# Kernel optimization log

Measured on AMD Instinct MI355X. Metric: run time of the kernel, lower is better.

The kernel has to match this reference:

```python
import jax, jax.numpy as jnp
import numpy as np

N_RAYS = 8192
AABB_LO, AABB_HI = -1.5, 1.5
GRID = 300
STEP_RATIO = 3.0
DIST_SCALE = 25.0
W_THRES = 1e-4
NEAR, FAR = 0.05, 6.0
NUM_SEM, DIM_INST = 20, 16
H_DEN, H_APP, F_APP, F_SEM = 64, 64, 27, 32

_EXT = AABB_HI - AABB_LO
STEP_SIZE = (_EXT / (GRID - 1 + 0.001)) * STEP_RATIO          # update_step_size
N_SAMPLES = int(np.sqrt(3.0) * _EXT / STEP_SIZE) + 1          # 173


def setup_inputs() -> dict:
    key = jax.random.key(0)
    ks = jax.random.split(key, 12)
    o = jax.random.normal(ks[0], (N_RAYS, 3), jnp.float32)
    o = 4.0 * o / jnp.linalg.norm(o, axis=-1, keepdims=True)      # camera origins on radius-4 sphere
    tgt = jax.random.uniform(ks[1], (N_RAYS, 3), jnp.float32, minval=-0.5, maxval=0.5)
    d = tgt - o
    d = d / jnp.linalg.norm(d, axis=-1, keepdims=True)            # unit viewdirs through the box
    rays = jnp.concatenate([o, d], -1)
    g = lambda k, shp, fan: jax.random.normal(k, shp, jnp.float32) / np.sqrt(fan)
    return {
        'rays': rays,
        'Wd1': g(ks[2], (3, H_DEN), 3), 'bd1': jnp.zeros((H_DEN,), jnp.float32),
        'Wd2': g(ks[3], (H_DEN, 1), H_DEN), 'bd2': jnp.zeros((1,), jnp.float32),
        'Wapp': g(ks[4], (3, F_APP), 3),
        'Wa1': g(ks[5], (F_APP + 3, H_APP), F_APP + 3), 'ba1': jnp.zeros((H_APP,), jnp.float32),
        'Wa2': g(ks[6], (H_APP, 3), H_APP), 'ba2': jnp.zeros((3,), jnp.float32),
        'Wsf': g(ks[7], (3, F_SEM), 3),
        'Wsm': g(ks[8], (F_SEM, NUM_SEM), F_SEM), 'bsm': jnp.zeros((NUM_SEM,), jnp.float32),
        'Wi': g(ks[9], (3, DIM_INST), 3),
        'perturb': 0, 'white_bg': 1, 'is_train': 0,
    }


def _render(rays, Wd1, bd1, Wd2, bd2, Wapp, Wa1, ba1, Wa2, ba2, Wsf, Wsm, bsm, Wi,
            white_bg):
    lo = jnp.full((3,), AABB_LO, rays.dtype)
    hi = jnp.full((3,), AABB_HI, rays.dtype)
    o, d = rays[:, :3], rays[:, 3:6]
    # --- sample_points_in_box (TensoRF sample_ray, perturb=0) ---
    vec = jnp.where(d == 0, 1e-6, d)
    rate_a = (hi - o) / vec
    rate_b = (lo - o) / vec
    t_min = jnp.clip(jnp.minimum(rate_a, rate_b).max(-1), NEAR, FAR)       # [N]
    rng = jnp.arange(N_SAMPLES, dtype=rays.dtype)
    z_vals = t_min[:, None] + rng[None, :] * STEP_SIZE                     # [N,S]
    xyz = o[:, None, :] + d[:, None, :] * z_vals[..., None]                # [N,S,3]
    mask_xyz = jnp.all((xyz >= lo) & (xyz <= hi), -1)                      # [N,S]
    dists = jnp.concatenate([z_vals[:, 1:] - z_vals[:, :-1],
                             jnp.zeros_like(z_vals[:, :1])], -1)
    mid = jnp.concatenate([(z_vals[:, 1:] + z_vals[:, :-1]) * 0.5,
                           z_vals[:, -2:-1]], -1)
    # --- normalize_coordinates ---
    xyzn = (xyz - lo) * (2.0 / _EXT) - 1.0
    # --- density (masked query -> dense compute + where, same values) ---
    h = jax.nn.relu(xyzn @ Wd1 + bd1)                                      # [N,S,Hd]
    sigma = jnp.where(mask_xyz, jax.nn.softplus((h @ Wd2 + bd2)[..., 0]), 0.0)
    # --- raw_to_alpha ---
    alpha = 1.0 - jnp.exp(-sigma * (dists * DIST_SCALE))                   # [N,S]
    T = jnp.cumprod(jnp.concatenate([jnp.ones_like(alpha[:, :1]),
                                     1.0 - alpha + 1e-10], -1), -1)
    weight = alpha * T[:, :-1]
    # --- eff_distloss(weight, mid, dists) ---
    loss_uni = (dists * weight * weight).sum(-1).mean() / 3.0
    wm = weight * mid
    w_cs = jnp.cumsum(weight, -1)
    wm_cs = jnp.cumsum(wm, -1)
    loss_bi = 2.0 * (wm[:, 1:] * w_cs[:, :-1] - weight[:, 1:] * wm_cs[:, :-1]).sum(-1).mean()
    dist_reg = loss_uni + loss_bi
    # --- appearance / semantics / instances on appearance_mask ---
    app_mask = weight > W_THRES
    viewdirs = jnp.broadcast_to(d[:, None, :], xyz.shape)
    feat = xyzn @ Wapp                                                     # [N,S,27]
    ha = jax.nn.relu(jnp.concatenate([feat, viewdirs], -1) @ Wa1 + ba1)    # [N,S,Ha]
    rgb = jnp.where(app_mask[..., None], jax.nn.sigmoid(ha @ Wa2 + ba2), 0.0)
    sem = jnp.where(app_mask[..., None], (xyzn @ Wsf) @ Wsm + bsm, 0.0)
    inst = jnp.where(app_mask[..., None], xyzn @ Wi, 0.0)
    # --- compositing ---
    opacity = weight.sum(-1)
    rgb_map = (weight[..., None] * rgb).sum(-2)
    depth_map = (weight * z_vals).sum(-1)
    w = jax.lax.stop_gradient(weight)[..., None]                           # stop_semantic_grad
    semantics = (w * sem).sum(-2)
    instances = (w * inst).sum(-2)                                          # is_train=False
    if white_bg:
        rgb_map = rgb_map + (1.0 - opacity[..., None])
    rgb_map = jnp.clip(rgb_map, 0.0, 1.0)
    return rgb_map, semantics, instances, depth_map, dist_reg


def reference(rays, Wd1, bd1, Wd2, bd2, Wapp, Wa1, ba1, Wa2, ba2, Wsf, Wsm, bsm, Wi,
              perturb, white_bg, is_train):
    return _render(rays, Wd1, bd1, Wd2, bd2, Wapp, Wa1, ba1, Wa2, ba2,
                   Wsf, Wsm, bsm, Wi, bool(white_bg))
```

## Files before the change

kernel.cpp:

```cpp
#include <hip/hip_runtime.h>

#define NRAYS 8192
#define NSAMP 173
#define LASTI 172
#define NBLK  (NRAYS / 4)

__device__ __forceinline__ float RL(float x, int u) {
    return __int_as_float(__builtin_amdgcn_readlane(__float_as_int(x), u));
}

template <int CTRL, int RM, bool BC>
__device__ __forceinline__ float updpp(float old, float x) {
    return __int_as_float(__builtin_amdgcn_update_dpp(
        __float_as_int(old), __float_as_int(x), CTRL, RM, 0xf, BC));
}

__device__ __forceinline__ float scan_add64(float x) {
    x += updpp<0x111, 0xf, true>(0.f, x);
    x += updpp<0x112, 0xf, true>(0.f, x);
    x += updpp<0x114, 0xf, true>(0.f, x);
    x += updpp<0x118, 0xf, true>(0.f, x);
    x += updpp<0x142, 0xa, true>(0.f, x);
    x += updpp<0x143, 0xc, true>(0.f, x);
    return x;
}

__device__ __forceinline__ float scan_mul64(float x) {
    x *= updpp<0x111, 0xf, false>(1.f, x);
    x *= updpp<0x112, 0xf, false>(1.f, x);
    x *= updpp<0x114, 0xf, false>(1.f, x);
    x *= updpp<0x118, 0xf, false>(1.f, x);
    x *= updpp<0x142, 0xa, false>(1.f, x);
    x *= updpp<0x143, 0xc, false>(1.f, x);
    return x;
}

__device__ __forceinline__ float wave_sum64(float v) {
    return RL(scan_add64(v), 63);
}

__device__ __forceinline__ float softplus_f(float x) {
    if (x > 15.f) return x;
    return __logf(1.f + __expf(x));
}
__device__ __forceinline__ float sigmoid_f(float x) {
    return 1.f / (1.f + __expf(-x));
}

__launch_bounds__(256, 4)
__global__ void render_kernel(
    const float* __restrict__ rays,
    const float* __restrict__ Wd1, const float* __restrict__ bd1,
    const float* __restrict__ Wd2, const float* __restrict__ bd2,
    const float* __restrict__ Wapp, const float* __restrict__ Wa1,
    const float* __restrict__ ba1, const float* __restrict__ Wa2,
    const float* __restrict__ ba2, const float* __restrict__ Wsf,
    const float* __restrict__ Wsm, const float* __restrict__ bsm,
    const float* __restrict__ Wi,
    const int* __restrict__ whitebg_p,
    float* __restrict__ out,
    float* __restrict__ wsdist)
{
    __shared__ float4 qd4[64];
    __shared__ float  wd2s[64];
    __shared__ float4 apAs[64];
    __shared__ float2 apBs[64];
    __shared__ float  wscs[60];
    __shared__ float  bsmS[20];

    const int t = threadIdx.x;
    const int wid = t >> 6, lane = t & 63;
    const int r = blockIdx.x * 4 + wid;

    if (t < 64) {
        qd4[t] = make_float4(Wd1[t], Wd1[64 + t], Wd1[128 + t], bd1[t]);
        wd2s[t] = Wd2[t];
    } else if (t < 128) {
        int u = t - 64;
        apBs[u] = make_float2(Wa2[3 * u + 1], Wa2[3 * u + 2]);
    } else if (t < 192) {
        int u = t - 128;
        float s0 = 0.f, s1 = 0.f, s2 = 0.f;
        for (int j = 0; j < 27; ++j) {
            float w = Wa1[j * 64 + u];
            s0 = fmaf(Wapp[j], w, s0);
            s1 = fmaf(Wapp[27 + j], w, s1);
            s2 = fmaf(Wapp[54 + j], w, s2);
        }
        apAs[u] = make_float4(s0, s1, s2, Wa2[3 * u]);
    } else {
        for (int job = t - 192; job < 80; job += 64) {
            if (job < 60) {
                int m = job / 20, s = job % 20;
                float a = 0.f;
                for (int k = 0; k < 32; ++k) a = fmaf(Wsf[m * 32 + k], Wsm[k * 20 + s], a);
                wscs[job] = a;
            } else {
                bsmS[job - 60] = bsm[job - 60];
            }
        }
    }

    const float o0 = rays[r * 6 + 0], o1 = rays[r * 6 + 1], o2 = rays[r * 6 + 2];
    const float d0 = rays[r * 6 + 3], d1 = rays[r * 6 + 4], d2 = rays[r * 6 + 5];

    float tm;
    {
        float v0 = (d0 == 0.f) ? 1e-6f : d0;
        float v1 = (d1 == 0.f) ? 1e-6f : d1;
        float v2 = (d2 == 0.f) ? 1e-6f : d2;
        float a0 = __fdiv_rn(__fsub_rn(1.5f, o0), v0), b0 = __fdiv_rn(__fsub_rn(-1.5f, o0), v0);
        float a1 = __fdiv_rn(__fsub_rn(1.5f, o1), v1), b1 = __fdiv_rn(__fsub_rn(-1.5f, o1), v1);
        float a2 = __fdiv_rn(__fsub_rn(1.5f, o2), v2), b2 = __fdiv_rn(__fsub_rn(-1.5f, o2), v2);
        float m0 = fminf(a0, b0), m1 = fminf(a1, b1), m2 = fminf(a2, b2);
        tm = fmaxf(fmaxf(m0, m1), m2);
        tm = fminf(fmaxf(tm, 0.05f), 6.0f);
    }

    float dcr;
    {
        float b = ba1[lane];
        b = fmaf(d0, Wa1[27 * 64 + lane], b);
        b = fmaf(d1, Wa1[28 * 64 + lane], b);
        b = fmaf(d2, Wa1[29 * 64 + lane], b);
        dcr = b;
    }

    const float bd2c = bd2[0];
    const float ba2c0 = ba2[0], ba2c1 = ba2[1], ba2c2 = ba2[2];

    __syncthreads();

    const float STEPF = (float)(3.0 / 299.001 * 3.0);
    const float zlast2 = __fadd_rn(tm, __fmul_rn(171.f, STEPF));

    float aR0 = 0.f, aR1 = 0.f, aR2 = 0.f;
    float aS0 = 0.f, aS1 = 0.f, aS2 = 0.f;
    float aSw = 0.f;
    float aD = 0.f, aLu = 0.f, aLb = 0.f;
    float Tc = 1.f, Wcar = 0.f, WMc = 0.f;

    for (int c = 0; c < 3; ++c) {
        int i = (c << 6) + lane;
        bool valid = i < NSAMP;
        float z = __fadd_rn(tm, __fmul_rn((float)i, STEPF));
        float x0 = __fadd_rn(o0, __fmul_rn(d0, z));
        float x1 = __fadd_rn(o1, __fmul_rn(d1, z));
        float x2 = __fadd_rn(o2, __fmul_rn(d2, z));
        bool inbox = valid && (x0 >= -1.5f) && (x0 <= 1.5f) && (x1 >= -1.5f) && (x1 <= 1.5f) &&
                     (x2 >= -1.5f) && (x2 <= 1.5f);
        if (__ballot(inbox) == 0ull) break;

        float xn0 = x0 * (2.f / 3.f), xn1 = x1 * (2.f / 3.f), xn2 = x2 * (2.f / 3.f);

        float sp = bd2c;
#pragma unroll 8
        for (int u = 0; u < 64; ++u) {
            float4 q = qd4[u];
            float h = fmaf(xn0, q.x, fmaf(xn1, q.y, fmaf(xn2, q.z, q.w)));
            sp = fmaf(fmaxf(h, 0.f), wd2s[u], sp);
        }
        float sigma = inbox ? softplus_f(sp) : 0.f;

        float znext = __fadd_rn(tm, __fmul_rn((float)(i + 1), STEPF));
        float dist = (i < LASTI) ? __fsub_rn(znext, z) : 0.f;
        float alpha = 1.f - __expf(-sigma * dist * 25.f);
        float f = 1.f - alpha + 1e-10f;

        float p = scan_mul64(f);
        float pex = updpp<0x138, 0xf, false>(1.f, p);
        float T = Tc * pex;
        float w = alpha * T;

        float mid = (i < LASTI) ? 0.5f * __fadd_rn(z, znext) : zlast2;
        float wm = w * mid;

        float sw = scan_add64(w);
        float swm = scan_add64(wm);
        float wex = updpp<0x138, 0xf, true>(0.f, sw);
        float wmex = updpp<0x138, 0xf, true>(0.f, swm);

        aLb += wm * (Wcar + wex) - w * (WMc + wmex);
        aLu = fmaf(dist * w, w, aLu);
        aD = fmaf(w, z, aD);

        Tc *= RL(p, 63);
        Wcar += RL(sw, 63);
        WMc += RL(swm, 63);

        float wapp = (w > 1e-4f) ? w : 0.f;
        if (__ballot(wapp > 0.f) != 0ull) {
            float c0 = 0.f, c1 = 0.f, c2 = 0.f;
#pragma unroll 8
            for (int u = 0; u < 64; ++u) {
                float4 A4 = apAs[u];
                float2 B2 = apBs[u];
                float dcu = RL(dcr, u);
                float h = fmaf(xn0, A4.x, fmaf(xn1, A4.y, fmaf(xn2, A4.z, dcu)));
                h = fmaxf(h, 0.f);
                c0 = fmaf(h, A4.w, c0);
                c1 = fmaf(h, B2.x, c1);
                c2 = fmaf(h, B2.y, c2);
            }
            aR0 = fmaf(wapp, sigmoid_f(c0 + ba2c0), aR0);
            aR1 = fmaf(wapp, sigmoid_f(c1 + ba2c1), aR1);
            aR2 = fmaf(wapp, sigmoid_f(c2 + ba2c2), aR2);
            aS0 = fmaf(wapp, xn0, aS0);
            aS1 = fmaf(wapp, xn1, aS1);
            aS2 = fmaf(wapp, xn2, aS2);
            aSw += wapp;
        }

        if (Tc < 1e-8f) break;
    }

    aR0 = wave_sum64(aR0); aR1 = wave_sum64(aR1); aR2 = wave_sum64(aR2);
    aS0 = wave_sum64(aS0); aS1 = wave_sum64(aS1); aS2 = wave_sum64(aS2);
    aSw = wave_sum64(aSw);
    aD = wave_sum64(aD);
    aLu = wave_sum64(aLu);
    aLb = wave_sum64(aLb);

    float opac = Wcar;
    int wb = *whitebg_p;
    float bg = wb ? (1.f - opac) : 0.f;

    float* out_rgb = out;
    float* out_sem = out + 24576;
    float* out_inst = out + 188416;
    float* out_dep = out + 319488;

    if (lane < 3) {
        float rv = (lane == 0 ? aR0 : (lane == 1 ? aR1 : aR2)) + bg;
        rv = fminf(fmaxf(rv, 0.f), 1.f);
        out_rgb[r * 3 + lane] = rv;
    }
    if (lane < 20) {
        float sv = aS0 * wscs[lane] + aS1 * wscs[20 + lane] + aS2 * wscs[40 + lane] +
                   aSw * bsmS[lane];
        out_sem[r * 20 + lane] = sv;
    }
    if (lane < 16) {
        float iv = aS0 * Wi[lane] + aS1 * Wi[16 + lane] + aS2 * Wi[32 + lane];
        out_inst[r * 16 + lane] = iv;
    }
    if (lane == 0) {
        out_dep[r] = aD;
        wsdist[r] = aLu * (1.f / 3.f) + 2.f * aLb;
    }
}

__global__ void reduce_dist_kernel(const float* __restrict__ ws, float* __restrict__ out) {
    __shared__ float sm[256];
    int t = threadIdx.x;
    float a = 0.f;
    const float4* w4 = (const float4*)ws;
    for (int i = t; i < NRAYS / 4; i += 256) {
        float4 v = w4[i];
        a += (v.x + v.y) + (v.z + v.w);
    }
    sm[t] = a;
    __syncthreads();
    for (int st = 128; st > 0; st >>= 1) {
        if (t < st) sm[t] += sm[t + st];
        __syncthreads();
    }
    if (t == 0) out[0] = sm[0] * (1.f / (float)NRAYS);
}

extern "C" void kernel_launch(void* const* d_in, const int* in_sizes, int n_in,
                              void* d_out, int out_size, void* d_ws, size_t ws_size,
                              hipStream_t stream) {
    const float* rays = (const float*)d_in[0];
    const float* Wd1  = (const float*)d_in[1];
    const float* bd1  = (const float*)d_in[2];
    const float* Wd2  = (const float*)d_in[3];
    const float* bd2  = (const float*)d_in[4];
    const float* Wapp = (const float*)d_in[5];
    const float* Wa1  = (const float*)d_in[6];
    const float* ba1  = (const float*)d_in[7];
    const float* Wa2  = (const float*)d_in[8];
    const float* ba2  = (const float*)d_in[9];
    const float* Wsf  = (const float*)d_in[10];
    const float* Wsm  = (const float*)d_in[11];
    const float* bsm  = (const float*)d_in[12];
    const float* Wi   = (const float*)d_in[13];
    const int* wb     = (const int*)d_in[15];

    float* out = (float*)d_out;
    float* wsd = (float*)d_ws;

    render_kernel<<<NBLK, 256, 0, stream>>>(rays, Wd1, bd1, Wd2, bd2, Wapp, Wa1, ba1,
                                            Wa2, ba2, Wsf, Wsm, bsm, Wi, wb, out, wsd);
    reduce_dist_kernel<<<1, 256, 0, stream>>>(wsd, out + 327680);
}
```

Measured before the change: 29.25 us.

## Fold ray origin and direction into per-ray linear coefficients for MLP hidden units

Since sample points lie on a ray, each first-layer hidden pre-activation is affine in z. The kernel now precomputes a per-wave slope and intercept for every hidden unit, for both the density MLP and the appearance MLP, and stores them in per-wave shared arrays. The inner loops then need one FMA per hidden unit instead of three, and the readlane broadcast goes away. The cost is an extra per-ray setup phase, larger shared memory, and slightly different floating-point rounding.

```diff
diff --git a/kernel.cpp b/kernel.cpp
--- a/kernel.cpp
+++ b/kernel.cpp
@@ -61,10 +61,10 @@
     float* __restrict__ out,
     float* __restrict__ wsdist)
 {
-    __shared__ float4 qd4[64];
-    __shared__ float  wd2s[64];
+    __shared__ float4 gkwD[4][64];
+    __shared__ float2 gkA[4][64];
+    __shared__ float4 bQ[64];
     __shared__ float4 apAs[64];
-    __shared__ float2 apBs[64];
     __shared__ float  wscs[60];
     __shared__ float  bsmS[20];
 
@@ -73,12 +73,8 @@
     const int r = blockIdx.x * 4 + wid;
 
     if (t < 64) {
-        qd4[t] = make_float4(Wd1[t], Wd1[64 + t], Wd1[128 + t], bd1[t]);
-        wd2s[t] = Wd2[t];
-    } else if (t < 128) {
-        int u = t - 64;
-        apBs[u] = make_float2(Wa2[3 * u + 1], Wa2[3 * u + 2]);
-    } else if (t < 192) {
+        bQ[t] = make_float4(Wa2[3 * t], Wa2[3 * t + 1], Wa2[3 * t + 2], 0.f);
+    } else if (t >= 128 && t < 192) {
         int u = t - 128;
         float s0 = 0.f, s1 = 0.f, s2 = 0.f;
         for (int j = 0; j < 27; ++j) {
@@ -87,8 +83,8 @@
             s1 = fmaf(Wapp[27 + j], w, s1);
             s2 = fmaf(Wapp[54 + j], w, s2);
         }
-        apAs[u] = make_float4(s0, s1, s2, Wa2[3 * u]);
-    } else {
+        apAs[u] = make_float4(s0, s1, s2, 0.f);
+    } else if (t >= 192) {
         for (int job = t - 192; job < 80; job += 64) {
             if (job < 60) {
                 int m = job / 20, s = job % 20;
@@ -117,19 +113,29 @@
         tm = fminf(fmaxf(tm, 0.05f), 6.0f);
     }
 
-    float dcr;
     {
-        float b = ba1[lane];
-        b = fmaf(d0, Wa1[27 * 64 + lane], b);
-        b = fmaf(d1, Wa1[28 * 64 + lane], b);
-        b = fmaf(d2, Wa1[29 * 64 + lane], b);
-        dcr = b;
+        float qx = Wd1[lane], qy = Wd1[64 + lane], qz = Wd1[128 + lane];
+        float qw = bd1[lane], w2 = Wd2[lane];
+        float gd = fmaf(d2, qz, fmaf(d1, qy, d0 * qx)) * (2.f / 3.f);
+        float kd = fmaf(fmaf(o2, qz, fmaf(o1, qy, o0 * qx)), (2.f / 3.f), qw);
+        gkwD[wid][lane] = make_float4(gd, kd, w2, 0.f);
     }
 
     const float bd2c = bd2[0];
     const float ba2c0 = ba2[0], ba2c1 = ba2[1], ba2c2 = ba2[2];
 
     __syncthreads();
+
+    {
+        float4 A = apAs[lane];
+        float dc = ba1[lane];
+        dc = fmaf(d0, Wa1[27 * 64 + lane], dc);
+        dc = fmaf(d1, Wa1[28 * 64 + lane], dc);
+        dc = fmaf(d2, Wa1[29 * 64 + lane], dc);
+        float ga = fmaf(d2, A.z, fmaf(d1, A.y, d0 * A.x)) * (2.f / 3.f);
+        float ka = fmaf(fmaf(o2, A.z, fmaf(o1, A.y, o0 * A.x)), (2.f / 3.f), dc);
+        gkA[wid][lane] = make_float2(ga, ka);
+    }
 
     const float STEPF = (float)(3.0 / 299.001 * 3.0);
     const float zlast2 = __fadd_rn(tm, __fmul_rn(171.f, STEPF));
@@ -156,9 +162,9 @@
         float sp = bd2c;
 #pragma unroll 8
         for (int u = 0; u < 64; ++u) {
-            float4 q = qd4[u];
-            float h = fmaf(xn0, q.x, fmaf(xn1, q.y, fmaf(xn2, q.z, q.w)));
-            sp = fmaf(fmaxf(h, 0.f), wd2s[u], sp);
+            float4 g = gkwD[wid][u];
+            float h = fmaf(z, g.x, g.y);
+            sp = fmaf(fmaxf(h, 0.f), g.z, sp);
         }
         float sigma = inbox ? softplus_f(sp) : 0.f;
 
@@ -193,14 +199,13 @@
             float c0 = 0.f, c1 = 0.f, c2 = 0.f;
 #pragma unroll 8
             for (int u = 0; u < 64; ++u) {
-                float4 A4 = apAs[u];
-                float2 B2 = apBs[u];
-                float dcu = RL(dcr, u);
-                float h = fmaf(xn0, A4.x, fmaf(xn1, A4.y, fmaf(xn2, A4.z, dcu)));
+                float2 g = gkA[wid][u];
+                float4 b = bQ[u];
+                float h = fmaf(z, g.x, g.y);
                 h = fmaxf(h, 0.f);
-                c0 = fmaf(h, A4.w, c0);
-                c1 = fmaf(h, B2.x, c1);
-                c2 = fmaf(h, B2.y, c2);
+                c0 = fmaf(h, b.x, c0);
+                c1 = fmaf(h, b.y, c1);
+                c2 = fmaf(h, b.z, c2);
             }
             aR0 = fmaf(wapp, sigmoid_f(c0 + ba2c0), aR0);
             aR1 = fmaf(wapp, sigmoid_f(c1 + ba2c1), aR1);
```

Result: slower. 32.49 us (+11.1%).

## Keep MLP weights in registers and broadcast via DPP row_newbcast inline asm

Applied to the files above, without the earlier changes.

Each lane now holds a 16-way slice of the density and appearance MLP weights in VGPRs, loaded once per wave. The per-sample hidden units are computed with v_fmac_f32_dpp row_newbcast, which broadcasts one register lane per row, replacing per-iteration LDS reads of weights and per-unit readlane of the direction bias. This removes LDS traffic and SGPR readlane serialization from the inner loops. The cost is more VGPRs, four partial accumulators that change summation order, and reliance on gfx950-specific DPP modes written in inline assembly.

```diff
diff --git a/kernel.cpp b/kernel.cpp
--- a/kernel.cpp
+++ b/kernel.cpp
@@ -46,6 +46,43 @@
 __device__ __forceinline__ float sigmoid_f(float x) {
     return 1.f / (1.f + __expf(-x));
 }
+
+#define RMASK " row_mask:0xf bank_mask:0xf"
+
+#define DEN1(S, N)                                                                    \
+    do {                                                                              \
+        float t_;                                                                     \
+        asm("v_mov_b32_dpp %[t], %[qw] row_newbcast:" #N RMASK "\n\t"                 \
+            "v_fmac_f32_dpp %[t], %[qx], %[x0] row_newbcast:" #N RMASK "\n\t"         \
+            "v_fmac_f32_dpp %[t], %[qy], %[x1] row_newbcast:" #N RMASK "\n\t"         \
+            "v_fmac_f32_dpp %[t], %[qz], %[x2] row_newbcast:" #N RMASK "\n\t"         \
+            "v_max_f32 %[t], 0, %[t]\n\t"                                             \
+            "v_fmac_f32_dpp %[sp], %[w2], %[t] row_newbcast:" #N RMASK                \
+            : [t] "=&v"(t_), [sp] "+v"(sps##S)                                        \
+            : [qw] "v"(qw[S]), [qx] "v"(qx[S]), [qy] "v"(qy[S]), [qz] "v"(qz[S]),     \
+              [w2] "v"(w2[S]), [x0] "v"(xn0), [x1] "v"(xn1), [x2] "v"(xn2));          \
+    } while (0)
+
+#define DEN4(N) DEN1(0, N); DEN1(1, N); DEN1(2, N); DEN1(3, N)
+
+#define APP1(S, N)                                                                    \
+    do {                                                                              \
+        float t_;                                                                     \
+        asm("v_mov_b32_dpp %[t], %[dcv] row_newbcast:" #N RMASK "\n\t"                \
+            "v_fmac_f32_dpp %[t], %[a0], %[x0] row_newbcast:" #N RMASK "\n\t"         \
+            "v_fmac_f32_dpp %[t], %[a1], %[x1] row_newbcast:" #N RMASK "\n\t"         \
+            "v_fmac_f32_dpp %[t], %[a2], %[x2] row_newbcast:" #N RMASK "\n\t"         \
+            "v_max_f32 %[t], 0, %[t]\n\t"                                             \
+            "v_fmac_f32_dpp %[c0], %[b0], %[t] row_newbcast:" #N RMASK "\n\t"         \
+            "v_fmac_f32_dpp %[c1], %[b1], %[t] row_newbcast:" #N RMASK "\n\t"         \
+            "v_fmac_f32_dpp %[c2], %[b2], %[t] row_newbcast:" #N RMASK                \
+            : [t] "=&v"(t_), [c0] "+v"(c0##S), [c1] "+v"(c1##S), [c2] "+v"(c2##S)     \
+            : [dcv] "v"(dc[S]), [a0] "v"(a0r[S]), [a1] "v"(a1r[S]), [a2] "v"(a2r[S]), \
+              [b0] "v"(b0r[S]), [b1] "v"(b1r[S]), [b2] "v"(b2r[S]),                   \
+              [x0] "v"(xn0), [x1] "v"(xn1), [x2] "v"(xn2));                           \
+    } while (0)
+
+#define APP4(N) APP1(0, N); APP1(1, N); APP1(2, N); APP1(3, N)
 
 __launch_bounds__(256, 4)
 __global__ void render_kernel(
@@ -70,6 +107,7 @@
 
     const int t = threadIdx.x;
     const int wid = t >> 6, lane = t & 63;
+    const int k = lane & 15;
     const int r = blockIdx.x * 4 + wid;
 
     if (t < 64) {
@@ -93,7 +131,7 @@
             if (job < 60) {
                 int m = job / 20, s = job % 20;
                 float a = 0.f;
-                for (int k = 0; k < 32; ++k) a = fmaf(Wsf[m * 32 + k], Wsm[k * 20 + s], a);
+                for (int kk = 0; kk < 32; ++kk) a = fmaf(Wsf[m * 32 + kk], Wsm[kk * 20 + s], a);
                 wscs[job] = a;
             } else {
                 bsmS[job - 60] = bsm[job - 60];
@@ -117,19 +155,29 @@
         tm = fminf(fmaxf(tm, 0.05f), 6.0f);
     }
 
-    float dcr;
-    {
-        float b = ba1[lane];
-        b = fmaf(d0, Wa1[27 * 64 + lane], b);
-        b = fmaf(d1, Wa1[28 * 64 + lane], b);
-        b = fmaf(d2, Wa1[29 * 64 + lane], b);
-        dcr = b;
-    }
-
     const float bd2c = bd2[0];
     const float ba2c0 = ba2[0], ba2c1 = ba2[1], ba2c2 = ba2[2];
 
     __syncthreads();
+
+    float qx[4], qy[4], qz[4], qw[4], w2[4];
+    float dc[4], a0r[4], a1r[4], a2r[4], b0r[4], b1r[4], b2r[4];
+#pragma unroll
+    for (int s = 0; s < 4; ++s) {
+        int idx = 16 * s + k;
+        float4 q = qd4[idx];
+        qx[s] = q.x; qy[s] = q.y; qz[s] = q.z; qw[s] = q.w;
+        w2[s] = wd2s[idx];
+        float4 A = apAs[idx];
+        a0r[s] = A.x; a1r[s] = A.y; a2r[s] = A.z; b0r[s] = A.w;
+        float2 B = apBs[idx];
+        b1r[s] = B.x; b2r[s] = B.y;
+        float b = ba1[idx];
+        b = fmaf(d0, Wa1[27 * 64 + idx], b);
+        b = fmaf(d1, Wa1[28 * 64 + idx], b);
+        b = fmaf(d2, Wa1[29 * 64 + idx], b);
+        dc[s] = b;
+    }
 
     const float STEPF = (float)(3.0 / 299.001 * 3.0);
     const float zlast2 = __fadd_rn(tm, __fmul_rn(171.f, STEPF));
@@ -153,14 +201,13 @@
 
         float xn0 = x0 * (2.f / 3.f), xn1 = x1 * (2.f / 3.f), xn2 = x2 * (2.f / 3.f);
 
-        float sp = bd2c;
-#pragma unroll 8
-        for (int u = 0; u < 64; ++u) {
-            float4 q = qd4[u];
-            float h = fmaf(xn0, q.x, fmaf(xn1, q.y, fmaf(xn2, q.z, q.w)));
-            sp = fmaf(fmaxf(h, 0.f), wd2s[u], sp);
-        }
-        float sigma = inbox ? softplus_f(sp) : 0.f;
+        float sps0 = bd2c, sps1 = 0.f, sps2 = 0.f, sps3 = 0.f;
+        DEN4(0);  DEN4(1);  DEN4(2);  DEN4(3);
+        DEN4(4);  DEN4(5);  DEN4(6);  DEN4(7);
+        DEN4(8);  DEN4(9);  DEN4(10); DEN4(11);
+        DEN4(12); DEN4(13); DEN4(14); DEN4(15);
+        float spv = (sps0 + sps1) + (sps2 + sps3);
+        float sigma = inbox ? softplus_f(spv) : 0.f;
 
         float znext = __fadd_rn(tm, __fmul_rn((float)(i + 1), STEPF));
         float dist = (i < LASTI) ? __fsub_rn(znext, z) : 0.f;
@@ -190,21 +237,19 @@
 
         float wapp = (w > 1e-4f) ? w : 0.f;
         if (__ballot(wapp > 0.f) != 0ull) {
-            float c0 = 0.f, c1 = 0.f, c2 = 0.f;
-#pragma unroll 8
-            for (int u = 0; u < 64; ++u) {
-                float4 A4 = apAs[u];
-                float2 B2 = apBs[u];
-                float dcu = RL(dcr, u);
-                float h = fmaf(xn0, A4.x, fmaf(xn1, A4.y, fmaf(xn2, A4.z, dcu)));
-                h = fmaxf(h, 0.f);
-                c0 = fmaf(h, A4.w, c0);
-                c1 = fmaf(h, B2.x, c1);
-                c2 = fmaf(h, B2.y, c2);
-            }
-            aR0 = fmaf(wapp, sigmoid_f(c0 + ba2c0), aR0);
-            aR1 = fmaf(wapp, sigmoid_f(c1 + ba2c1), aR1);
-            aR2 = fmaf(wapp, sigmoid_f(c2 + ba2c2), aR2);
+            float c00 = 0.f, c01 = 0.f, c02 = 0.f, c03 = 0.f;
+            float c10 = 0.f, c11 = 0.f, c12 = 0.f, c13 = 0.f;
+            float c20 = 0.f, c21 = 0.f, c22 = 0.f, c23 = 0.f;
+            APP4(0);  APP4(1);  APP4(2);  APP4(3);
+            APP4(4);  APP4(5);  APP4(6);  APP4(7);
+            APP4(8);  APP4(9);  APP4(10); APP4(11);
+            APP4(12); APP4(13); APP4(14); APP4(15);
+            float c0v = (c00 + c01) + (c02 + c03);
+            float c1v = (c10 + c11) + (c12 + c13);
+            float c2v = (c20 + c21) + (c22 + c23);
+            aR0 = fmaf(wapp, sigmoid_f(c0v + ba2c0), aR0);
+            aR1 = fmaf(wapp, sigmoid_f(c1v + ba2c1), aR1);
+            aR2 = fmaf(wapp, sigmoid_f(c2v + ba2c2), aR2);
             aS0 = fmaf(wapp, xn0, aS0);
             aS1 = fmaf(wapp, xn1, aS1);
             aS2 = fmaf(wapp, xn2, aS2);
```

New measurement: 32.56 us. 1.11x slower.
